# Optimization experiments

Hardware: AMD Instinct MI355X
Metric: run time of the kernel (lower is better)

The kernel has to match this reference:

```python
import jax, jax.numpy as jnp
import numpy as np

LN_EPS = 1e-5


def setup_inputs() -> dict:
    key = jax.random.key(0)
    k1, k2, k3 = jax.random.split(key, 3)
    N, E, D_IN, D_OUT = 50000, 500000, 128, 128
    x = jax.random.normal(k1, (N, D_IN), dtype=jnp.float32)
    edge_index = jax.random.randint(k2, (2, E), 0, N, dtype=jnp.int64)
    W = jax.random.normal(k3, (D_IN, D_OUT), dtype=jnp.float32) * (1.0 / np.sqrt(D_IN))
    b = jnp.zeros((D_OUT,), dtype=jnp.float32)
    ln_gamma = jnp.ones((D_OUT,), dtype=jnp.float32)
    ln_beta = jnp.zeros((D_OUT,), dtype=jnp.float32)
    return {"x": x, "edge_index": edge_index, "W": W, "b": b,
            "ln_gamma": ln_gamma, "ln_beta": ln_beta}


def reference(x, edge_index, W, b, ln_gamma, ln_beta):
    N = x.shape[0]
    # GCNConv: linear transform first (no fused bias; bias added after aggregation)
    h = x @ W  # [N, D_out]
    # add self-loops
    loops = jnp.arange(N, dtype=edge_index.dtype)
    src = jnp.concatenate([edge_index[0], loops])  # [E+N]
    dst = jnp.concatenate([edge_index[1], loops])  # [E+N]
    # symmetric normalization deg^{-1/2} (degree computed on dst, incl. self-loops)
    deg = jax.ops.segment_sum(jnp.ones(src.shape, dtype=h.dtype), dst, num_segments=N)
    dinv = jnp.where(deg > 0, jax.lax.rsqrt(deg), 0.0)
    norm = dinv[src] * dinv[dst]  # [E+N]
    # gather messages, scale, scatter-add to destinations
    msgs = h[src] * norm[:, None]  # [E+N, D_out]
    out = jax.ops.segment_sum(msgs, dst, num_segments=N) + b  # [N, D_out]
    # LayerNorm over features
    mu = out.mean(axis=-1, keepdims=True)
    var = out.var(axis=-1, keepdims=True)
    out = (out - mu) * jax.lax.rsqrt(var + LN_EPS) * ln_gamma + ln_beta
    # activation
    return jax.nn.relu(out)
```

## Files before the change

### kernel.cpp

```cpp
#include <hip/hip_runtime.h>
#include <hip/hip_fp16.h>
#include <math.h>

#define D 128
#define LN_EPS 1e-5f
#define BKT 64

typedef _Float16 f16x8 __attribute__((ext_vector_type(8)));
typedef float    f32x4 __attribute__((ext_vector_type(4)));

__global__ void prep_kernel(const float* __restrict__ W, _Float16* __restrict__ wtg,
                            int* __restrict__ degi, int N) {
    int idx = blockIdx.x * 256 + threadIdx.x;
    int k = idx >> 7;
    int n = idx & 127;
    wtg[n * D + k] = (_Float16)W[k * D + n];
    for (int i = idx; i < N; i += 64 * 256) degi[i] = 0;
}

__global__ void fused_kernel(const float* __restrict__ x, const _Float16* __restrict__ wtg,
                             unsigned* __restrict__ h2,
                             const int* __restrict__ src, const int* __restrict__ dst,
                             int* __restrict__ degi, int* __restrict__ bucket,
                             int N, int E, int nbG) {
    __shared__ _Float16 xs[64][136];
    int tid = threadIdx.x;

    if ((int)blockIdx.x >= nbG) {
        int e = (blockIdx.x - nbG) * 256 + tid;
        if (e < E) {
            int d = dst[e];
            int p = atomicAdd(&degi[d], 1);
            if (p < BKT) bucket[(size_t)d * BKT + p] = src[e];
        }
        return;
    }

    int row0 = blockIdx.x * 64;
#pragma unroll
    for (int i = 0; i < 8; ++i) {
        int idx = i * 256 + tid;
        int r   = idx >> 5;
        int c4  = idx & 31;
        float4 v = make_float4(0.f, 0.f, 0.f, 0.f);
        if (row0 + r < N) v = *(const float4*)&x[(size_t)(row0 + r) * D + c4 * 4];
        __half2 lo = __floats2half2_rn(v.x, v.y);
        __half2 hi = __floats2half2_rn(v.z, v.w);
        *(__half2*)&xs[r][c4 * 4]     = lo;
        *(__half2*)&xs[r][c4 * 4 + 2] = hi;
    }
    __syncthreads();

    int l     = tid & 63;
    int mtile = tid >> 6;
    int mn    = l & 15;
    int kq    = (l >> 4) * 8;
    f32x4 acc[8];
#pragma unroll
    for (int nt = 0; nt < 8; ++nt) acc[nt] = (f32x4){0.f, 0.f, 0.f, 0.f};

#pragma unroll
    for (int ks = 0; ks < 4; ++ks) {
        int kb = ks * 32 + kq;
        f16x8 a = *(f16x8*)&xs[mtile * 16 + mn][kb];
#pragma unroll
        for (int nt = 0; nt < 8; ++nt) {
            f16x8 bf = *(const f16x8*)&wtg[(nt * 16 + mn) * D + kb];
            acc[nt] = __builtin_amdgcn_mfma_f32_16x16x32_f16(a, bf, acc[nt], 0, 0, 0);
        }
    }

    int quad = l >> 4;
#pragma unroll
    for (int nt = 0; nt < 8; ++nt) {
#pragma unroll
        for (int rg = 0; rg < 4; ++rg) {
            float v  = acc[nt][rg];
            float pv = __shfl_xor(v, 1);
            if (!(l & 1)) {
                int row = row0 + mtile * 16 + quad * 4 + rg;
                if (row < N) {
                    __half2 p = __floats2half2_rn(v, pv);
                    h2[(size_t)row * (D / 2) + nt * 8 + (mn >> 1)] = *(unsigned*)&p;
                }
            }
        }
    }
}

__device__ __forceinline__ void acc_edge(float& a0, float& a1, unsigned u, float w) {
    __half2 hv = *(__half2*)&u;
    a0 = fmaf(__low2float(hv),  w, a0);
    a1 = fmaf(__high2float(hv), w, a1);
}

__global__ void gather_ln_kernel(const int* __restrict__ bucket, const int* __restrict__ degi,
                                 const unsigned* __restrict__ h2, const float* __restrict__ b,
                                 const float* __restrict__ g, const float* __restrict__ be,
                                 float* __restrict__ out, int N) {
    int row  = blockIdx.x * 4 + (threadIdx.x >> 6);
    int lane = threadIdx.x & 63;
    if (row >= N) return;
    int dg   = degi[row];
    int dgc  = dg < BKT ? dg : BKT;
    float di = rsqrtf((float)dg + 1.0f);
    float sw = di * di;
    unsigned su = h2[(size_t)row * (D / 2) + lane];
    float acc0 = 0.f, acc1 = 0.f;
    acc_edge(acc0, acc1, su, sw);
    const int* bk = bucket + (size_t)row * BKT;

    int e = 0;
    for (; e + 8 <= dgc; e += 8) {
        int4 ra = *(const int4*)&bk[e];
        int4 rb = *(const int4*)&bk[e + 4];
        int s[8] = {ra.x, ra.y, ra.z, ra.w, rb.x, rb.y, rb.z, rb.w};
        unsigned u[8]; float wgt[8];
#pragma unroll
        for (int j = 0; j < 8; ++j) u[j] = h2[(size_t)s[j] * (D / 2) + lane];
#pragma unroll
        for (int j = 0; j < 8; ++j) wgt[j] = rsqrtf((float)degi[s[j]] + 1.0f) * di;
#pragma unroll
        for (int j = 0; j < 8; ++j) acc_edge(acc0, acc1, u[j], wgt[j]);
    }
    int rem = dgc - e;
    if (rem & 4) {
        int4 ra = *(const int4*)&bk[e];
        int s[4] = {ra.x, ra.y, ra.z, ra.w};
        unsigned u[4]; float wgt[4];
#pragma unroll
        for (int j = 0; j < 4; ++j) u[j] = h2[(size_t)s[j] * (D / 2) + lane];
#pragma unroll
        for (int j = 0; j < 4; ++j) wgt[j] = rsqrtf((float)degi[s[j]] + 1.0f) * di;
#pragma unroll
        for (int j = 0; j < 4; ++j) acc_edge(acc0, acc1, u[j], wgt[j]);
        e += 4;
    }
    if (rem & 2) {
        int s0 = bk[e], s1 = bk[e + 1];
        unsigned u0 = h2[(size_t)s0 * (D / 2) + lane];
        unsigned u1 = h2[(size_t)s1 * (D / 2) + lane];
        float w0 = rsqrtf((float)degi[s0] + 1.0f) * di;
        float w1 = rsqrtf((float)degi[s1] + 1.0f) * di;
        acc_edge(acc0, acc1, u0, w0);
        acc_edge(acc0, acc1, u1, w1);
        e += 2;
    }
    if (rem & 1) {
        int s0 = bk[e];
        unsigned u0 = h2[(size_t)s0 * (D / 2) + lane];
        float w0 = rsqrtf((float)degi[s0] + 1.0f) * di;
        acc_edge(acc0, acc1, u0, w0);
    }

    float2 bb = *(const float2*)&b[lane * 2];
    float v0 = acc0 + bb.x;
    float v1 = acc1 + bb.y;
    float s = v0 + v1;
    float q = v0 * v0 + v1 * v1;
#pragma unroll
    for (int off = 32; off; off >>= 1) {
        s += __shfl_xor(s, off);
        q += __shfl_xor(q, off);
    }
    float mean = s * (1.0f / 128.0f);
    float var  = q * (1.0f / 128.0f) - mean * mean;
    float rstd = rsqrtf(var + LN_EPS);
    float2 gg = *(const float2*)&g[lane * 2];
    float2 eb = *(const float2*)&be[lane * 2];
    float y0 = (v0 - mean) * rstd * gg.x + eb.x;
    float y1 = (v1 - mean) * rstd * gg.y + eb.y;
    *(float2*)&out[(size_t)row * D + lane * 2] = make_float2(fmaxf(y0, 0.0f), fmaxf(y1, 0.0f));
}

extern "C" void kernel_launch(void* const* d_in, const int* in_sizes, int n_in,
                              void* d_out, int out_size, void* d_ws, size_t ws_size,
                              hipStream_t stream) {
    const float* x  = (const float*)d_in[0];
    const int*   ei = (const int*)d_in[1];
    const float* W  = (const float*)d_in[2];
    const float* b  = (const float*)d_in[3];
    const float* g  = (const float*)d_in[4];
    const float* be = (const float*)d_in[5];

    int N = in_sizes[0] / D;
    int E = in_sizes[1] / 2;
    const int* src = ei;
    const int* dst = ei + E;

    float* out = (float*)d_out;

    char* w = (char*)d_ws;
    unsigned* h2    = (unsigned*)w;           w += (size_t)N * (D / 2) * sizeof(unsigned);
    int*      degi  = (int*)w;                w += (size_t)N * sizeof(int);
    _Float16* wtg   = (_Float16*)w;           w += (size_t)D * D * sizeof(_Float16);
    int*      bucket= (int*)w;                w += (size_t)N * BKT * sizeof(int);

    int nbG = (N + 63) / 64;
    int nbB = (E + 255) / 256;

    prep_kernel <<<64,        256, 0, stream>>>(W, wtg, degi, N);
    fused_kernel<<<nbG + nbB, 256, 0, stream>>>(x, wtg, h2, src, dst, degi, bucket,
                                                N, E, nbG);
    gather_ln_kernel<<<(N + 3) / 4, 256, 0, stream>>>(bucket, degi, h2,
                                                      b, g, be, out, N);
}
```

Before: 144.8 us.

## Process two rows per wave in gather and batch four edges per bucket thread

The gather+LayerNorm kernel now gives each wavefront two rows, prefetching both rows' degree, first eight bucket entries and self features up front, then running the first 8-edge batch of each row before the remaining batches. The aim is more memory-level parallelism per wave to hide gather latency. The bucketing blocks also handle four edges per thread, cutting block count. Costs are more registers (lower occupancy) and the unconditional read of the first eight bucket slots even for low-degree rows.

Measured after the change: 147.8 us. +2.1%, slower.

```diff
diff --git a/kernel.cpp b/kernel.cpp
--- a/kernel.cpp
+++ b/kernel.cpp
@@ -27,11 +27,15 @@
     int tid = threadIdx.x;
 
     if ((int)blockIdx.x >= nbG) {
-        int e = (blockIdx.x - nbG) * 256 + tid;
-        if (e < E) {
-            int d = dst[e];
-            int p = atomicAdd(&degi[d], 1);
-            if (p < BKT) bucket[(size_t)d * BKT + p] = src[e];
+        int base = (blockIdx.x - nbG) * 1024 + tid;
+#pragma unroll
+        for (int k = 0; k < 4; ++k) {
+            int e = base + k * 256;
+            if (e < E) {
+                int d = dst[e];
+                int p = atomicAdd(&degi[d], 1);
+                if (p < BKT) bucket[(size_t)d * BKT + p] = src[e];
+            }
         }
         return;
     }
@@ -94,23 +98,10 @@
     a1 = fmaf(__high2float(hv), w, a1);
 }
 
-__global__ void gather_ln_kernel(const int* __restrict__ bucket, const int* __restrict__ degi,
-                                 const unsigned* __restrict__ h2, const float* __restrict__ b,
-                                 const float* __restrict__ g, const float* __restrict__ be,
-                                 float* __restrict__ out, int N) {
-    int row  = blockIdx.x * 4 + (threadIdx.x >> 6);
-    int lane = threadIdx.x & 63;
-    if (row >= N) return;
-    int dg   = degi[row];
-    int dgc  = dg < BKT ? dg : BKT;
-    float di = rsqrtf((float)dg + 1.0f);
-    float sw = di * di;
-    unsigned su = h2[(size_t)row * (D / 2) + lane];
-    float acc0 = 0.f, acc1 = 0.f;
-    acc_edge(acc0, acc1, su, sw);
-    const int* bk = bucket + (size_t)row * BKT;
-
-    int e = 0;
+__device__ __forceinline__ void row_batches(const int* __restrict__ bk, int dgc, int e,
+                                            const int* __restrict__ degi,
+                                            const unsigned* __restrict__ h2,
+                                            int lane, float di, float& a0, float& a1) {
     for (; e + 8 <= dgc; e += 8) {
         int4 ra = *(const int4*)&bk[e];
         int4 rb = *(const int4*)&bk[e + 4];
@@ -121,7 +112,7 @@
 #pragma unroll
         for (int j = 0; j < 8; ++j) wgt[j] = rsqrtf((float)degi[s[j]] + 1.0f) * di;
 #pragma unroll
-        for (int j = 0; j < 8; ++j) acc_edge(acc0, acc1, u[j], wgt[j]);
+        for (int j = 0; j < 8; ++j) acc_edge(a0, a1, u[j], wgt[j]);
     }
     int rem = dgc - e;
     if (rem & 4) {
@@ -133,7 +124,7 @@
 #pragma unroll
         for (int j = 0; j < 4; ++j) wgt[j] = rsqrtf((float)degi[s[j]] + 1.0f) * di;
 #pragma unroll
-        for (int j = 0; j < 4; ++j) acc_edge(acc0, acc1, u[j], wgt[j]);
+        for (int j = 0; j < 4; ++j) acc_edge(a0, a1, u[j], wgt[j]);
         e += 4;
     }
     if (rem & 2) {
@@ -142,20 +133,22 @@
         unsigned u1 = h2[(size_t)s1 * (D / 2) + lane];
         float w0 = rsqrtf((float)degi[s0] + 1.0f) * di;
         float w1 = rsqrtf((float)degi[s1] + 1.0f) * di;
-        acc_edge(acc0, acc1, u0, w0);
-        acc_edge(acc0, acc1, u1, w1);
+        acc_edge(a0, a1, u0, w0);
+        acc_edge(a0, a1, u1, w1);
         e += 2;
     }
     if (rem & 1) {
         int s0 = bk[e];
         unsigned u0 = h2[(size_t)s0 * (D / 2) + lane];
         float w0 = rsqrtf((float)degi[s0] + 1.0f) * di;
-        acc_edge(acc0, acc1, u0, w0);
-    }
-
-    float2 bb = *(const float2*)&b[lane * 2];
-    float v0 = acc0 + bb.x;
-    float v1 = acc1 + bb.y;
+        acc_edge(a0, a1, u0, w0);
+    }
+}
+
+__device__ __forceinline__ void row_epilogue(float v0, float v1, int lane, int row,
+                                             const float* __restrict__ g,
+                                             const float* __restrict__ be,
+                                             float* __restrict__ out) {
     float s = v0 + v1;
     float q = v0 * v0 + v1 * v1;
 #pragma unroll
@@ -171,6 +164,70 @@
     float y0 = (v0 - mean) * rstd * gg.x + eb.x;
     float y1 = (v1 - mean) * rstd * gg.y + eb.y;
     *(float2*)&out[(size_t)row * D + lane * 2] = make_float2(fmaxf(y0, 0.0f), fmaxf(y1, 0.0f));
+}
+
+__global__ void gather_ln_kernel(const int* __restrict__ bucket, const int* __restrict__ degi,
+                                 const unsigned* __restrict__ h2, const float* __restrict__ b,
+                                 const float* __restrict__ g, const float* __restrict__ be,
+                                 float* __restrict__ out, int N) {
+    int wave = threadIdx.x >> 6;
+    int lane = threadIdx.x & 63;
+    int rowA = blockIdx.x * 8 + wave * 2;
+    if (rowA >= N) return;
+    int rowB = rowA + 1;
+    bool hasB = rowB < N;
+    int rB = hasB ? rowB : rowA;
+
+    int dgA = degi[rowA];
+    int dgB = degi[rB];
+    const int* bkA = bucket + (size_t)rowA * BKT;
+    const int* bkB = bucket + (size_t)rB * BKT;
+    int4 pa0 = *(const int4*)&bkA[0];
+    int4 pa1 = *(const int4*)&bkA[4];
+    int4 pb0 = *(const int4*)&bkB[0];
+    int4 pb1 = *(const int4*)&bkB[4];
+    unsigned suA = h2[(size_t)rowA * (D / 2) + lane];
+    unsigned suB = h2[(size_t)rB * (D / 2) + lane];
+
+    int dgcA = dgA < BKT ? dgA : BKT;
+    int dgcB = dgB < BKT ? dgB : BKT;
+    float diA = rsqrtf((float)dgA + 1.0f);
+    float diB = rsqrtf((float)dgB + 1.0f);
+
+    float a0 = 0.f, a1 = 0.f, b0 = 0.f, b1 = 0.f;
+    acc_edge(a0, a1, suA, diA * diA);
+    acc_edge(b0, b1, suB, diB * diB);
+
+    int eA = 0, eB = 0;
+    if (dgcA >= 8) {
+        int s[8] = {pa0.x, pa0.y, pa0.z, pa0.w, pa1.x, pa1.y, pa1.z, pa1.w};
+        unsigned u[8]; float wgt[8];
+#pragma unroll
+        for (int j = 0; j < 8; ++j) u[j] = h2[(size_t)s[j] * (D / 2) + lane];
+#pragma unroll
+        for (int j = 0; j < 8; ++j) wgt[j] = rsqrtf((float)degi[s[j]] + 1.0f) * diA;
+#pragma unroll
+        for (int j = 0; j < 8; ++j) acc_edge(a0, a1, u[j], wgt[j]);
+        eA = 8;
+    }
+    if (dgcB >= 8) {
+        int s[8] = {pb0.x, pb0.y, pb0.z, pb0.w, pb1.x, pb1.y, pb1.z, pb1.w};
+        unsigned u[8]; float wgt[8];
+#pragma unroll
+        for (int j = 0; j < 8; ++j) u[j] = h2[(size_t)s[j] * (D / 2) + lane];
+#pragma unroll
+        for (int j = 0; j < 8; ++j) wgt[j] = rsqrtf((float)degi[s[j]] + 1.0f) * diB;
+#pragma unroll
+        for (int j = 0; j < 8; ++j) acc_edge(b0, b1, u[j], wgt[j]);
+        eB = 8;
+    }
+
+    row_batches(bkA, dgcA, eA, degi, h2, lane, diA, a0, a1);
+    row_batches(bkB, dgcB, eB, degi, h2, lane, diB, b0, b1);
+
+    float2 bb = *(const float2*)&b[lane * 2];
+    row_epilogue(a0 + bb.x, a1 + bb.y, lane, rowA, g, be, out);
+    if (hasB) row_epilogue(b0 + bb.x, b1 + bb.y, lane, rowB, g, be, out);
 }
 
 extern "C" void kernel_launch(void* const* d_in, const int* in_sizes, int n_in,
@@ -197,11 +254,11 @@
     int*      bucket= (int*)w;                w += (size_t)N * BKT * sizeof(int);
 
     int nbG = (N + 63) / 64;
-    int nbB = (E + 255) / 256;
+    int nbB = (E + 1023) / 1024;
 
     prep_kernel <<<64,        256, 0, stream>>>(W, wtg, degi, N);
     fused_kernel<<<nbG + nbB, 256, 0, stream>>>(x, wtg, h2, src, dst, degi, bucket,
                                                 N, E, nbG);
-    gather_ln_kernel<<<(N + 3) / 4, 256, 0, stream>>>(bucket, degi, h2,
+    gather_ln_kernel<<<(N + 7) / 8, 256, 0, stream>>>(bucket, degi, h2,
                                                       b, g, be, out, N);
 }
```

## Gather two rows per wave with 8-byte loads; batch bucket edges per block

Applied to the files above, without the earlier changes.

The gather/LayerNorm kernel now assigns each half-wave one row, with each lane loading four fp16 features (uint2) instead of two. This halves the number of waves and doubles the bytes per load per row, so more independent gathers are in flight. The LN reduction shrinks to a 32-lane shuffle and the stores become float4. In the fused kernel, bucket blocks are moved before the GEMM blocks and each handles 1024 edges, which cuts block count and makes the atomic bucketing start earlier.

Measured after the change: 153.1 us. 1.06x slower.

```diff
diff --git a/kernel.cpp b/kernel.cpp
--- a/kernel.cpp
+++ b/kernel.cpp
@@ -22,21 +22,25 @@
                              unsigned* __restrict__ h2,
                              const int* __restrict__ src, const int* __restrict__ dst,
                              int* __restrict__ degi, int* __restrict__ bucket,
-                             int N, int E, int nbG) {
+                             int N, int E, int nbB) {
     __shared__ _Float16 xs[64][136];
     int tid = threadIdx.x;
 
-    if ((int)blockIdx.x >= nbG) {
-        int e = (blockIdx.x - nbG) * 256 + tid;
-        if (e < E) {
-            int d = dst[e];
-            int p = atomicAdd(&degi[d], 1);
-            if (p < BKT) bucket[(size_t)d * BKT + p] = src[e];
+    if ((int)blockIdx.x < nbB) {
+        int base = blockIdx.x * 1024 + tid;
+#pragma unroll
+        for (int k = 0; k < 4; ++k) {
+            int e = base + k * 256;
+            if (e < E) {
+                int d = dst[e];
+                int p = atomicAdd(&degi[d], 1);
+                if (p < BKT) bucket[(size_t)d * BKT + p] = src[e];
+            }
         }
         return;
     }
 
-    int row0 = blockIdx.x * 64;
+    int row0 = (blockIdx.x - nbB) * 64;
 #pragma unroll
     for (int i = 0; i < 8; ++i) {
         int idx = i * 256 + tid;
@@ -88,89 +92,102 @@
     }
 }
 
-__device__ __forceinline__ void acc_edge(float& a0, float& a1, unsigned u, float w) {
-    __half2 hv = *(__half2*)&u;
-    a0 = fmaf(__low2float(hv),  w, a0);
-    a1 = fmaf(__high2float(hv), w, a1);
+__device__ __forceinline__ void acc4(float& a0, float& a1, float& a2, float& a3,
+                                     uint2 u, float w) {
+    __half2 h01 = *(__half2*)&u.x;
+    __half2 h23 = *(__half2*)&u.y;
+    a0 = fmaf(__low2float(h01),  w, a0);
+    a1 = fmaf(__high2float(h01), w, a1);
+    a2 = fmaf(__low2float(h23),  w, a2);
+    a3 = fmaf(__high2float(h23), w, a3);
 }
 
 __global__ void gather_ln_kernel(const int* __restrict__ bucket, const int* __restrict__ degi,
-                                 const unsigned* __restrict__ h2, const float* __restrict__ b,
+                                 const uint2* __restrict__ h4, const float* __restrict__ b,
                                  const float* __restrict__ g, const float* __restrict__ be,
                                  float* __restrict__ out, int N) {
-    int row  = blockIdx.x * 4 + (threadIdx.x >> 6);
+    int wave = threadIdx.x >> 6;
     int lane = threadIdx.x & 63;
-    if (row >= N) return;
-    int dg   = degi[row];
+    int half = lane >> 5;
+    int hl   = lane & 31;
+    int row  = blockIdx.x * 8 + wave * 2 + half;
+    bool valid = row < N;
+    int rr = valid ? row : N - 1;
+
+    int dg   = degi[rr];
     int dgc  = dg < BKT ? dg : BKT;
     float di = rsqrtf((float)dg + 1.0f);
-    float sw = di * di;
-    unsigned su = h2[(size_t)row * (D / 2) + lane];
-    float acc0 = 0.f, acc1 = 0.f;
-    acc_edge(acc0, acc1, su, sw);
-    const int* bk = bucket + (size_t)row * BKT;
+    const int* bk = bucket + (size_t)rr * BKT;
+
+    uint2 su = h4[(size_t)rr * 32 + hl];
+    float a0 = 0.f, a1 = 0.f, a2 = 0.f, a3 = 0.f;
+    acc4(a0, a1, a2, a3, su, di * di);
 
     int e = 0;
     for (; e + 8 <= dgc; e += 8) {
         int4 ra = *(const int4*)&bk[e];
         int4 rb = *(const int4*)&bk[e + 4];
         int s[8] = {ra.x, ra.y, ra.z, ra.w, rb.x, rb.y, rb.z, rb.w};
-        unsigned u[8]; float wgt[8];
-#pragma unroll
-        for (int j = 0; j < 8; ++j) u[j] = h2[(size_t)s[j] * (D / 2) + lane];
+        uint2 u[8]; float wgt[8];
+#pragma unroll
+        for (int j = 0; j < 8; ++j) u[j] = h4[(size_t)s[j] * 32 + hl];
 #pragma unroll
         for (int j = 0; j < 8; ++j) wgt[j] = rsqrtf((float)degi[s[j]] + 1.0f) * di;
 #pragma unroll
-        for (int j = 0; j < 8; ++j) acc_edge(acc0, acc1, u[j], wgt[j]);
+        for (int j = 0; j < 8; ++j) acc4(a0, a1, a2, a3, u[j], wgt[j]);
     }
     int rem = dgc - e;
     if (rem & 4) {
         int4 ra = *(const int4*)&bk[e];
         int s[4] = {ra.x, ra.y, ra.z, ra.w};
-        unsigned u[4]; float wgt[4];
-#pragma unroll
-        for (int j = 0; j < 4; ++j) u[j] = h2[(size_t)s[j] * (D / 2) + lane];
+        uint2 u[4]; float wgt[4];
+#pragma unroll
+        for (int j = 0; j < 4; ++j) u[j] = h4[(size_t)s[j] * 32 + hl];
 #pragma unroll
         for (int j = 0; j < 4; ++j) wgt[j] = rsqrtf((float)degi[s[j]] + 1.0f) * di;
 #pragma unroll
-        for (int j = 0; j < 4; ++j) acc_edge(acc0, acc1, u[j], wgt[j]);
+        for (int j = 0; j < 4; ++j) acc4(a0, a1, a2, a3, u[j], wgt[j]);
         e += 4;
     }
     if (rem & 2) {
         int s0 = bk[e], s1 = bk[e + 1];
-        unsigned u0 = h2[(size_t)s0 * (D / 2) + lane];
-        unsigned u1 = h2[(size_t)s1 * (D / 2) + lane];
+        uint2 u0 = h4[(size_t)s0 * 32 + hl];
+        uint2 u1 = h4[(size_t)s1 * 32 + hl];
         float w0 = rsqrtf((float)degi[s0] + 1.0f) * di;
         float w1 = rsqrtf((float)degi[s1] + 1.0f) * di;
-        acc_edge(acc0, acc1, u0, w0);
-        acc_edge(acc0, acc1, u1, w1);
+        acc4(a0, a1, a2, a3, u0, w0);
+        acc4(a0, a1, a2, a3, u1, w1);
         e += 2;
     }
     if (rem & 1) {
         int s0 = bk[e];
-        unsigned u0 = h2[(size_t)s0 * (D / 2) + lane];
+        uint2 u0 = h4[(size_t)s0 * 32 + hl];
         float w0 = rsqrtf((float)degi[s0] + 1.0f) * di;
-        acc_edge(acc0, acc1, u0, w0);
-    }
-
-    float2 bb = *(const float2*)&b[lane * 2];
-    float v0 = acc0 + bb.x;
-    float v1 = acc1 + bb.y;
-    float s = v0 + v1;
-    float q = v0 * v0 + v1 * v1;
-#pragma unroll
-    for (int off = 32; off; off >>= 1) {
+        acc4(a0, a1, a2, a3, u0, w0);
+    }
+
+    float4 bb = *(const float4*)&b[hl * 4];
+    float v0 = a0 + bb.x, v1 = a1 + bb.y, v2 = a2 + bb.z, v3 = a3 + bb.w;
+    float s = v0 + v1 + v2 + v3;
+    float q = v0 * v0 + v1 * v1 + v2 * v2 + v3 * v3;
+#pragma unroll
+    for (int off = 16; off; off >>= 1) {
         s += __shfl_xor(s, off);
         q += __shfl_xor(q, off);
     }
     float mean = s * (1.0f / 128.0f);
     float var  = q * (1.0f / 128.0f) - mean * mean;
     float rstd = rsqrtf(var + LN_EPS);
-    float2 gg = *(const float2*)&g[lane * 2];
-    float2 eb = *(const float2*)&be[lane * 2];
-    float y0 = (v0 - mean) * rstd * gg.x + eb.x;
-    float y1 = (v1 - mean) * rstd * gg.y + eb.y;
-    *(float2*)&out[(size_t)row * D + lane * 2] = make_float2(fmaxf(y0, 0.0f), fmaxf(y1, 0.0f));
+    float4 gg = *(const float4*)&g[hl * 4];
+    float4 eb = *(const float4*)&be[hl * 4];
+    if (valid) {
+        float4 y;
+        y.x = fmaxf((v0 - mean) * rstd * gg.x + eb.x, 0.0f);
+        y.y = fmaxf((v1 - mean) * rstd * gg.y + eb.y, 0.0f);
+        y.z = fmaxf((v2 - mean) * rstd * gg.z + eb.z, 0.0f);
+        y.w = fmaxf((v3 - mean) * rstd * gg.w + eb.w, 0.0f);
+        *(float4*)&out[(size_t)row * D + hl * 4] = y;
+    }
 }
 
 extern "C" void kernel_launch(void* const* d_in, const int* in_sizes, int n_in,
@@ -197,11 +214,11 @@
     int*      bucket= (int*)w;                w += (size_t)N * BKT * sizeof(int);
 
     int nbG = (N + 63) / 64;
-    int nbB = (E + 255) / 256;
+    int nbB = (E + 1023) / 1024;
 
     prep_kernel <<<64,        256, 0, stream>>>(W, wtg, degi, N);
-    fused_kernel<<<nbG + nbB, 256, 0, stream>>>(x, wtg, h2, src, dst, degi, bucket,
-                                                N, E, nbG);
-    gather_ln_kernel<<<(N + 3) / 4, 256, 0, stream>>>(bucket, degi, h2,
+    fused_kernel<<<nbB + nbG, 256, 0, stream>>>(x, wtg, h2, src, dst, degi, bucket,
+                                                N, E, nbB);
+    gather_ln_kernel<<<(N + 7) / 8, 256, 0, stream>>>(bucket, degi, (const uint2*)h2,
                                                       b, g, be, out, N);
 }
```

## Prescale features by source dinv and unconditionally gather first 16 neighbors

Applied to the files above, without the earlier changes.

Adds a pass that multiplies each node's fp16 features by its own deg^-1/2, written to a padded buffer with a zero sentinel row. The gather then drops the per-edge degi lookup and rsqrt, applying the destination dinv once at the end. It also pre-fills the first 16 bucket slots of every row with the sentinel index so the first 16 neighbor loads can be issued unconditionally for more memory parallelism. The costs are an extra kernel launch, an extra N×256-byte write and read, a sentinel fill of bucket memory in prep, and an additional fp16 rounding after the dinv scaling.

After: 155.0 us. +7.1%, slower.

```diff
diff --git a/kernel.cpp b/kernel.cpp
--- a/kernel.cpp
+++ b/kernel.cpp
@@ -9,13 +9,23 @@
 typedef _Float16 f16x8 __attribute__((ext_vector_type(8)));
 typedef float    f32x4 __attribute__((ext_vector_type(4)));
 
+__device__ __forceinline__ int clampN(int s, int N) {
+    return (int)min((unsigned)s, (unsigned)N);
+}
+
 __global__ void prep_kernel(const float* __restrict__ W, _Float16* __restrict__ wtg,
-                            int* __restrict__ degi, int N) {
+                            int* __restrict__ degi, int4* __restrict__ bkt4, int N) {
     int idx = blockIdx.x * 256 + threadIdx.x;
-    int k = idx >> 7;
-    int n = idx & 127;
-    wtg[n * D + k] = (_Float16)W[k * D + n];
-    for (int i = idx; i < N; i += 64 * 256) degi[i] = 0;
+    if (idx < 16384) {
+        int k = idx >> 7, n = idx & 127;
+        wtg[n * D + k] = (_Float16)W[k * D + n];
+    }
+    for (int i = idx; i < N; i += 65536) degi[i] = 0;
+    int4 sv = make_int4(N, N, N, N);
+    for (int i = idx; i < N * 4; i += 65536) {
+        int row = i >> 2, q = i & 3;
+        bkt4[(size_t)row * 16 + q] = sv;
+    }
 }
 
 __global__ void fused_kernel(const float* __restrict__ x, const _Float16* __restrict__ wtg,
@@ -30,8 +40,11 @@
         int e = (blockIdx.x - nbG) * 256 + tid;
         if (e < E) {
             int d = dst[e];
-            int p = atomicAdd(&degi[d], 1);
-            if (p < BKT) bucket[(size_t)d * BKT + p] = src[e];
+            int s = src[e];
+            if ((unsigned)d < (unsigned)N && (unsigned)s < (unsigned)N) {
+                int p = atomicAdd(&degi[d], 1);
+                if (p < BKT) bucket[(size_t)d * BKT + p] = s;
+            }
         }
         return;
     }
@@ -88,14 +101,22 @@
     }
 }
 
-__device__ __forceinline__ void acc_edge(float& a0, float& a1, unsigned u, float w) {
-    __half2 hv = *(__half2*)&u;
-    a0 = fmaf(__low2float(hv),  w, a0);
-    a1 = fmaf(__high2float(hv), w, a1);
+__global__ void hw_kernel(const unsigned* __restrict__ h2, const int* __restrict__ degi,
+                          unsigned* __restrict__ hw2, int N) {
+    int idx = blockIdx.x * 256 + threadIdx.x;
+    int total = (N + 1) * 64;
+    if (idx >= total) return;
+    int row = idx >> 6;
+    if (row >= N) { hw2[idx] = 0u; return; }
+    float di = rsqrtf((float)degi[row] + 1.0f);
+    unsigned uu = h2[idx];
+    __half2 hv = *(__half2*)&uu;
+    __half2 p  = __floats2half2_rn(__low2float(hv) * di, __high2float(hv) * di);
+    hw2[idx] = *(unsigned*)&p;
 }
 
 __global__ void gather_ln_kernel(const int* __restrict__ bucket, const int* __restrict__ degi,
-                                 const unsigned* __restrict__ h2, const float* __restrict__ b,
+                                 const unsigned* __restrict__ hw2, const float* __restrict__ b,
                                  const float* __restrict__ g, const float* __restrict__ be,
                                  float* __restrict__ out, int N) {
     int row  = blockIdx.x * 4 + (threadIdx.x >> 6);
@@ -103,67 +124,99 @@
     if (row >= N) return;
     int dg   = degi[row];
     int dgc  = dg < BKT ? dg : BKT;
+    if (dgc < 0) dgc = 0;
     float di = rsqrtf((float)dg + 1.0f);
-    float sw = di * di;
-    unsigned su = h2[(size_t)row * (D / 2) + lane];
-    float acc0 = 0.f, acc1 = 0.f;
-    acc_edge(acc0, acc1, su, sw);
     const int* bk = bucket + (size_t)row * BKT;
 
-    int e = 0;
+    int4 q0 = *(const int4*)&bk[0];
+    int4 q1 = *(const int4*)&bk[4];
+    int4 q2 = *(const int4*)&bk[8];
+    int4 q3 = *(const int4*)&bk[12];
+    unsigned su = hw2[(size_t)row * 64 + lane];
+
+    int s[16] = {q0.x, q0.y, q0.z, q0.w, q1.x, q1.y, q1.z, q1.w,
+                 q2.x, q2.y, q2.z, q2.w, q3.x, q3.y, q3.z, q3.w};
+    unsigned u[16];
+#pragma unroll
+    for (int j = 0; j < 16; ++j) s[j] = clampN(s[j], N);
+#pragma unroll
+    for (int j = 0; j < 16; ++j) u[j] = hw2[(size_t)s[j] * 64 + lane];
+
+    float acc0, acc1;
+    {
+        __half2 hv = *(__half2*)&su;
+        acc0 = __low2float(hv);
+        acc1 = __high2float(hv);
+    }
+#pragma unroll
+    for (int j = 0; j < 16; ++j) {
+        __half2 hv = *(__half2*)&u[j];
+        acc0 += __low2float(hv);
+        acc1 += __high2float(hv);
+    }
+
+    int e = 16;
     for (; e + 8 <= dgc; e += 8) {
         int4 ra = *(const int4*)&bk[e];
         int4 rb = *(const int4*)&bk[e + 4];
-        int s[8] = {ra.x, ra.y, ra.z, ra.w, rb.x, rb.y, rb.z, rb.w};
-        unsigned u[8]; float wgt[8];
-#pragma unroll
-        for (int j = 0; j < 8; ++j) u[j] = h2[(size_t)s[j] * (D / 2) + lane];
-#pragma unroll
-        for (int j = 0; j < 8; ++j) wgt[j] = rsqrtf((float)degi[s[j]] + 1.0f) * di;
-#pragma unroll
-        for (int j = 0; j < 8; ++j) acc_edge(acc0, acc1, u[j], wgt[j]);
+        int st[8] = {ra.x, ra.y, ra.z, ra.w, rb.x, rb.y, rb.z, rb.w};
+        unsigned ut[8];
+#pragma unroll
+        for (int j = 0; j < 8; ++j) st[j] = clampN(st[j], N);
+#pragma unroll
+        for (int j = 0; j < 8; ++j) ut[j] = hw2[(size_t)st[j] * 64 + lane];
+#pragma unroll
+        for (int j = 0; j < 8; ++j) {
+            __half2 hv = *(__half2*)&ut[j];
+            acc0 += __low2float(hv);
+            acc1 += __high2float(hv);
+        }
     }
     int rem = dgc - e;
     if (rem & 4) {
         int4 ra = *(const int4*)&bk[e];
-        int s[4] = {ra.x, ra.y, ra.z, ra.w};
-        unsigned u[4]; float wgt[4];
-#pragma unroll
-        for (int j = 0; j < 4; ++j) u[j] = h2[(size_t)s[j] * (D / 2) + lane];
-#pragma unroll
-        for (int j = 0; j < 4; ++j) wgt[j] = rsqrtf((float)degi[s[j]] + 1.0f) * di;
-#pragma unroll
-        for (int j = 0; j < 4; ++j) acc_edge(acc0, acc1, u[j], wgt[j]);
+        int st[4] = {ra.x, ra.y, ra.z, ra.w};
+        unsigned ut[4];
+#pragma unroll
+        for (int j = 0; j < 4; ++j) st[j] = clampN(st[j], N);
+#pragma unroll
+        for (int j = 0; j < 4; ++j) ut[j] = hw2[(size_t)st[j] * 64 + lane];
+#pragma unroll
+        for (int j = 0; j < 4; ++j) {
+            __half2 hv = *(__half2*)&ut[j];
+            acc0 += __low2float(hv);
+            acc1 += __high2float(hv);
+        }
         e += 4;
     }
     if (rem & 2) {
-        int s0 = bk[e], s1 = bk[e + 1];
-        unsigned u0 = h2[(size_t)s0 * (D / 2) + lane];
-        unsigned u1 = h2[(size_t)s1 * (D / 2) + lane];
-        float w0 = rsqrtf((float)degi[s0] + 1.0f) * di;
-        float w1 = rsqrtf((float)degi[s1] + 1.0f) * di;
-        acc_edge(acc0, acc1, u0, w0);
-        acc_edge(acc0, acc1, u1, w1);
+        int s0 = clampN(bk[e], N), s1 = clampN(bk[e + 1], N);
+        unsigned u0 = hw2[(size_t)s0 * 64 + lane];
+        unsigned u1 = hw2[(size_t)s1 * 64 + lane];
+        __half2 h0 = *(__half2*)&u0, h1 = *(__half2*)&u1;
+        acc0 += __low2float(h0) + __low2float(h1);
+        acc1 += __high2float(h0) + __high2float(h1);
         e += 2;
     }
     if (rem & 1) {
-        int s0 = bk[e];
-        unsigned u0 = h2[(size_t)s0 * (D / 2) + lane];
-        float w0 = rsqrtf((float)degi[s0] + 1.0f) * di;
-        acc_edge(acc0, acc1, u0, w0);
+        int s0 = clampN(bk[e], N);
+        unsigned u0 = hw2[(size_t)s0 * 64 + lane];
+        __half2 h0 = *(__half2*)&u0;
+        acc0 += __low2float(h0);
+        acc1 += __high2float(h0);
     }
 
     float2 bb = *(const float2*)&b[lane * 2];
-    float v0 = acc0 + bb.x;
-    float v1 = acc1 + bb.y;
-    float s = v0 + v1;
+    float v0 = acc0 * di + bb.x;
+    float v1 = acc1 * di + bb.y;
+    float sum = v0 + v1;
     float q = v0 * v0 + v1 * v1;
 #pragma unroll
     for (int off = 32; off; off >>= 1) {
-        s += __shfl_xor(s, off);
-        q += __shfl_xor(q, off);
-    }
-    float mean = s * (1.0f / 128.0f);
+        sum += __shfl_xor(sum, off);
+        q   += __shfl_xor(q, off);
+    }
+    float mean = sum * (1.0f / 128.0f);
     float var  = q * (1.0f / 128.0f) - mean * mean;
     float rstd = rsqrtf(var + LN_EPS);
     float2 gg = *(const float2*)&g[lane * 2];
@@ -192,16 +245,19 @@
 
     char* w = (char*)d_ws;
     unsigned* h2    = (unsigned*)w;           w += (size_t)N * (D / 2) * sizeof(unsigned);
+    unsigned* hw2   = (unsigned*)w;           w += (size_t)(N + 1) * (D / 2) * sizeof(unsigned);
     int*      degi  = (int*)w;                w += (size_t)N * sizeof(int);
     _Float16* wtg   = (_Float16*)w;           w += (size_t)D * D * sizeof(_Float16);
     int*      bucket= (int*)w;                w += (size_t)N * BKT * sizeof(int);
 
     int nbG = (N + 63) / 64;
     int nbB = (E + 255) / 256;
-
-    prep_kernel <<<64,        256, 0, stream>>>(W, wtg, degi, N);
+    int nHW = ((N + 1) * 64 + 255) / 256;
+
+    prep_kernel <<<256,       256, 0, stream>>>(W, wtg, degi, (int4*)bucket, N);
     fused_kernel<<<nbG + nbB, 256, 0, stream>>>(x, wtg, h2, src, dst, degi, bucket,
                                                 N, E, nbG);
-    gather_ln_kernel<<<(N + 3) / 4, 256, 0, stream>>>(bucket, degi, h2,
+    hw_kernel   <<<nHW,       256, 0, stream>>>(h2, degi, hw2, N);
+    gather_ln_kernel<<<(N + 3) / 4, 256, 0, stream>>>(bucket, degi, hw2,
                                                       b, g, be, out, N);
 }
```
